# Kernel optimization log

Measured on AMD Instinct MI355X. Metric: run time of the kernel, lower is better.

Reference implementation:

```python
import jax, jax.numpy as jnp
import numpy as np

D_MODEL = 1024
N_HEADS = 16
D_FF = 4096
EPS = 1e-5


def setup_inputs() -> dict:
    key = jax.random.key(0)
    ks = jax.random.split(key, 10)
    sig_attn = (1.0 / D_MODEL) ** 0.5
    sig1 = (2.0 / (D_MODEL + D_FF)) ** 0.5
    sig2 = (2.0 / (D_FF + D_MODEL)) ** 0.5
    return {
        "x": jax.random.normal(ks[0], (4, 2048, D_MODEL), dtype=jnp.float32),
        "W_q": jax.random.normal(ks[1], (D_MODEL, D_MODEL), jnp.float32) * sig_attn,
        "W_k": jax.random.normal(ks[2], (D_MODEL, D_MODEL), jnp.float32) * sig_attn,
        "W_v": jax.random.normal(ks[3], (D_MODEL, D_MODEL), jnp.float32) * sig_attn,
        "W_o": jax.random.normal(ks[4], (D_MODEL, D_MODEL), jnp.float32) * sig_attn,
        "gamma1": jnp.ones((D_MODEL,), jnp.float32),
        "gamma2": jnp.ones((D_MODEL,), jnp.float32),
        "W1": jax.random.normal(ks[5], (D_FF, D_MODEL), jnp.float32) * sig1,  # gate proj
        "W2": jax.random.normal(ks[6], (D_MODEL, D_FF), jnp.float32) * sig2,  # down proj
        "W3": jax.random.normal(ks[7], (D_FF, D_MODEL), jnp.float32) * sig1,  # up proj
    }


def _rmsnorm(x, gamma, eps=EPS):
    # computed in fp32 as in the original, cast back to input dtype
    in_dtype = x.dtype
    xf = x.astype(jnp.float32)
    norm = jnp.sqrt(jnp.mean(xf * xf, axis=-1, keepdims=True) + eps)
    return ((xf / norm) * gamma).astype(in_dtype)


def _mha(x, W_q, W_k, W_v, W_o, n_heads=N_HEADS):
    B, S, D = x.shape
    d_h = D // n_heads
    # projections: weights stored as [d_out, d_in]
    q = jnp.einsum('bsd,ed->bse', x, W_q).reshape(B, S, n_heads, d_h).transpose(0, 2, 1, 3)
    k = jnp.einsum('bsd,ed->bse', x, W_k).reshape(B, S, n_heads, d_h).transpose(0, 2, 1, 3)
    v = jnp.einsum('bsd,ed->bse', x, W_v).reshape(B, S, n_heads, d_h).transpose(0, 2, 1, 3)
    scores = jnp.einsum('bhqd,bhkd->bhqk', q, k) / jnp.sqrt(jnp.asarray(d_h, x.dtype))
    causal = jnp.tril(jnp.ones((S, S), dtype=bool))  # True = keep
    scores = jnp.where(causal, scores, -jnp.inf)
    probs = jax.nn.softmax(scores, axis=-1)
    out = jnp.einsum('bhqk,bhkd->bhqd', probs, v)
    out = out.transpose(0, 2, 1, 3).reshape(B, S, D)
    return jnp.einsum('bse,de->bsd', out, W_o)


def _swiglu(x, W1, W2, W3):
    g = jnp.einsum('bsd,fd->bsf', x, W1)
    u = jnp.einsum('bsd,fd->bsf', x, W3)
    return jnp.einsum('bsf,df->bsd', jax.nn.silu(g) * u, W2)


def reference(x, W_q, W_k, W_v, W_o, gamma1, gamma2, W1, W2, W3):
    x = x + _mha(_rmsnorm(x, gamma1), W_q, W_k, W_v, W_o)
    x = x + _swiglu(_rmsnorm(x, gamma2), W1, W2, W3)
    return x
```

## Files before the change

kernel.cpp:

```cpp
#include <hip/hip_runtime.h>
#include <cstdint>
#include <cstddef>

typedef unsigned short u16;
typedef unsigned int u32;
typedef short bf16x8 __attribute__((ext_vector_type(8)));
typedef float f32x4 __attribute__((ext_vector_type(4)));
typedef float f32x16 __attribute__((ext_vector_type(16)));
typedef u16 u16x4 __attribute__((ext_vector_type(4)));

__device__ __forceinline__ u16 f2bf(float f) {
  u32 u = __float_as_uint(f);
  return (u16)((u + 0x7FFFu + ((u >> 16) & 1u)) >> 16);
}
__device__ __forceinline__ float bf2f(u16 h) {
  return __uint_as_float(((u32)h) << 16);
}
__device__ __forceinline__ u32 cvtpk(float lo, float hi) {
  u32 r;
  asm("v_cvt_pk_bf16_f32 %0, %1, %2" : "=v"(r) : "v"(lo), "v"(hi));
  return r;
}
__device__ __forceinline__ float exp2a(float x) {
  float r;
  asm("v_exp_f32 %0, %1" : "=v"(r) : "v"(x));
  return r;
}

__device__ __forceinline__ void gload_lds16(const void* g, void* l) {
  __builtin_amdgcn_global_load_lds((const __attribute__((address_space(1))) u32*)g,
                                   (__attribute__((address_space(3))) u32*)l, 16, 0, 0);
}

__global__ __launch_bounds__(256) void castw_multi(
    const float* __restrict__ Wq, const float* __restrict__ Wk,
    const float* __restrict__ Wv, const float* __restrict__ Wo,
    const float* __restrict__ W2, u16* __restrict__ qkvw,
    u16* __restrict__ Wo_b, u16* __restrict__ W2_b) {
  const int bid = blockIdx.x;
  const float* src;
  u16x4* dst;
  int i;
  if (bid < 3072) {
    src = (bid < 1024) ? Wq : (bid < 2048) ? Wk : Wv;
    dst = (u16x4*)qkvw + (bid >> 10) * 262144;
    i = (bid & 1023) * 256 + threadIdx.x;
  } else if (bid < 4096) {
    src = Wo;
    dst = (u16x4*)Wo_b;
    i = (bid - 3072) * 256 + threadIdx.x;
  } else {
    src = W2;
    dst = (u16x4*)W2_b;
    i = (bid - 4096) * 256 + threadIdx.x;
  }
  float4 v = ((const float4*)src)[i];
  u16x4 r;
  r.x = f2bf(v.x); r.y = f2bf(v.y); r.z = f2bf(v.z); r.w = f2bf(v.w);
  dst[i] = r;
}

__global__ __launch_bounds__(256) void castw_pack2(const float* __restrict__ W1,
                                                   const float* __restrict__ W3,
                                                   u16* __restrict__ dst) {
  const int half = blockIdx.y;
  const float* src = half ? W3 : W1;
  int i = blockIdx.x * 256 + threadIdx.x;
  float4 v = ((const float4*)src)[i];
  const int n = i >> 8;
  const int c4 = i & 255;
  const int orow = ((n >> 6) << 7) + (half << 6) + (n & 63);
  u16x4 r;
  r.x = f2bf(v.x); r.y = f2bf(v.y); r.z = f2bf(v.z); r.w = f2bf(v.w);
  ((u16x4*)dst)[orow * 256 + c4] = r;
}

__global__ __launch_bounds__(256) void rmsnorm_k(const float* __restrict__ x,
                                                 const float* __restrict__ gamma,
                                                 u16* __restrict__ o) {
  const int row = blockIdx.x;
  const int t = threadIdx.x;
  float4 v = ((const float4*)(x + (size_t)row * 1024))[t];
  float ss = v.x * v.x + v.y * v.y + v.z * v.z + v.w * v.w;
  #pragma unroll
  for (int m = 1; m < 64; m <<= 1) ss += __shfl_xor(ss, m);
  __shared__ float wsum[4];
  if ((t & 63) == 0) wsum[t >> 6] = ss;
  __syncthreads();
  float tot = wsum[0] + wsum[1] + wsum[2] + wsum[3];
  float inv = rsqrtf(tot * (1.0f / 1024.0f) + 1e-5f);
  float4 g = ((const float4*)gamma)[t];
  u16x4 r;
  r.x = f2bf(v.x * inv * g.x);
  r.y = f2bf(v.y * inv * g.y);
  r.z = f2bf(v.z * inv * g.z);
  r.w = f2bf(v.w * inv * g.w);
  ((u16x4*)(o + (size_t)row * 1024))[t] = r;
}

template <int EPI>
__global__ __launch_bounds__(256, 4)
void gemm128(const u16* __restrict__ A, const u16* __restrict__ B,
             void* out, const void* ep, int M, int N, int KLOOP, int KS,
             float scale, int ncut) {
  __shared__ u16 smem[2][8192];
  u16* const sA = smem[0];
  u16* const sB = smem[1];

  const int tid = threadIdx.x;
  const int lane = tid & 63;
  const int w = tid >> 6;
  const int wr = w >> 1, wc = w & 1;
  const int lr = lane & 15, lk = lane >> 4;

  A += (size_t)blockIdx.z * KLOOP;
  B += (size_t)blockIdx.z * KLOOP;

  const int nx = gridDim.x;
  const int nwg = nx * gridDim.y;
  const int flat = blockIdx.y * nx + blockIdx.x;
  const int qq = nwg >> 3, rr = nwg & 7;
  const int xcd = flat & 7, off = flat >> 3;
  const int swz = (xcd < rr ? xcd * (qq + 1) : rr * (qq + 1) + (xcd - rr) * qq) + off;
  const int sr = nx * 8;
  const int g8 = swz / sr, rem = swz % sr;
  const int grp = rem >> 6, r6 = rem & 63;
  const int m0 = (g8 * 8 + (r6 & 7)) * 128;
  const int n0 = (grp * 8 + (r6 >> 3)) * 128;

  f32x4 acc[4][4];
  #pragma unroll
  for (int i = 0; i < 4; i++)
    #pragma unroll
    for (int j = 0; j < 4; j++) acc[i][j] = (f32x4){0.f, 0.f, 0.f, 0.f};

  for (int kt = 0; kt < KLOOP; kt += 64) {
    __syncthreads();
    #pragma unroll
    for (int r = 0; r < 4; r++) {
      const int q = r * 256 + tid;
      const int row = q >> 3;
      const int cs = (q & 7) ^ (row & 7);
      gload_lds16(A + (size_t)(m0 + row) * KS + kt + cs * 8, (char*)sA + q * 16);
      gload_lds16(B + (size_t)(n0 + row) * KS + kt + cs * 8, (char*)sB + q * 16);
    }
    __syncthreads();
    #pragma unroll
    for (int kk = 0; kk < 2; kk++) {
      bf16x8 a_[4], b_[4];
      #pragma unroll
      for (int i = 0; i < 4; i++)
        a_[i] = *(const bf16x8*)&sA[(wr * 64 + i * 16 + lr) * 64 +
                                    (((kk * 4 + lk) ^ (lr & 7)) * 8)];
      #pragma unroll
      for (int j = 0; j < 4; j++)
        b_[j] = *(const bf16x8*)&sB[(wc * 64 + j * 16 + lr) * 64 +
                                    (((kk * 4 + lk) ^ (lr & 7)) * 8)];
      #pragma unroll
      for (int i = 0; i < 4; i++)
        #pragma unroll
        for (int j = 0; j < 4; j++)
          acc[i][j] = __builtin_amdgcn_mfma_f32_16x16x32_bf16(a_[i], b_[j], acc[i][j], 0, 0, 0);
    }
  }

  if constexpr (EPI == 1 || EPI == 3) {
    #pragma unroll
    for (int i = 0; i < 4; i++)
      #pragma unroll
      for (int j = 0; j < 4; j++)
        #pragma unroll
        for (int r = 0; r < 4; r++) {
          const int grow = m0 + wr * 64 + i * 16 + lk * 4 + r;
          const int gcol = n0 + wc * 64 + j * 16 + lr;
          const size_t idx = (size_t)grow * N + gcol;
          if (EPI == 1) ((float*)out)[idx] = ((const float*)ep)[idx] + acc[i][j][r];
          else          unsafeAtomicAdd((float*)out + idx, acc[i][j][r]);
        }
  } else {
    bool vpath = false;
    if constexpr (EPI == 5) vpath = (n0 >= 2048);
    if (vpath) {
      u16* const smT = smem[0];
      __syncthreads();
      #pragma unroll
      for (int i = 0; i < 4; i++)
        #pragma unroll
        for (int j = 0; j < 4; j++)
          #pragma unroll
          for (int r = 0; r < 4; r++) {
            const int row = wr * 64 + i * 16 + lk * 4 + r;
            const int col = wc * 64 + j * 16 + lr;
            smT[col * 128 + (row ^ ((col & 7) << 3))] = f2bf(acc[i][j][r]);
          }
      __syncthreads();
      u16* const vt = (u16*)const_cast<void*>(ep);
      const int b = m0 >> 11;
      const int sbase = m0 & 2047;
      #pragma unroll
      for (int it = 0; it < 8; it++) {
        const int fl = it * 256 + tid;
        const int trow = fl >> 4;
        const int tch = fl & 15;
        bf16x8 cv = *(const bf16x8*)&smT[trow * 128 + ((tch * 8) ^ ((trow & 7) << 3))];
        const int dg = n0 - 2048 + trow;
        const int h = dg >> 6, d = dg & 63;
        *(bf16x8*)(vt + (((size_t)(b * 16 + h) * 64 + d) * 2048 + sbase + tch * 8)) = cv;
      }
    } else {
      u16* const smC = smem[0];
      const float s = ((EPI == 0 || EPI == 5) && n0 < ncut) ? scale : 1.0f;
      __syncthreads();
      #pragma unroll
      for (int i = 0; i < 4; i++)
        #pragma unroll
        for (int j = 0; j < 4; j++)
          #pragma unroll
          for (int r = 0; r < 4; r++) {
            const int row = wr * 64 + i * 16 + lk * 4 + r;
            const int col = wc * 64 + j * 16 + lr;
            smC[row * 128 + (col ^ ((row & 7) << 3))] = f2bf(acc[i][j][r] * s);
          }
      __syncthreads();
      if constexpr (EPI == 4) {
        #pragma unroll
        for (int it = 0; it < 4; it++) {
          const int fl = it * 256 + tid;
          const int row = fl >> 3;
          const int ch = fl & 7;
          bf16x8 gvv = *(const bf16x8*)&smC[row * 128 + ((ch ^ (row & 7)) * 8)];
          bf16x8 uvv = *(const bf16x8*)&smC[row * 128 + (((ch + 8) ^ (row & 7)) * 8)];
          bf16x8 ov;
          #pragma unroll
          for (int k = 0; k < 8; k++) {
            float g = bf2f((u16)gvv[k]);
            float u = bf2f((u16)uvv[k]);
            float sg = g / (1.f + __expf(-g));
            ov[k] = (short)f2bf(sg * u);
          }
          *(bf16x8*)((u16*)out + (size_t)(m0 + row) * N + (n0 >> 1) + ch * 8) = ov;
        }
      } else {
        #pragma unroll
        for (int it = 0; it < 8; it++) {
          const int fl = it * 256 + tid;
          const int row = fl >> 4;
          const int ch = fl & 15;
          bf16x8 cv = *(const bf16x8*)&smC[row * 128 + ((ch ^ (row & 7)) * 8)];
          const size_t gidx = (size_t)(m0 + row) * N + n0 + ch * 8;
          *(bf16x8*)((u16*)out + gidx) = cv;
        }
      }
    }
  }
}

__global__ __launch_bounds__(256, 4)
void attn_fwd5(const u16* __restrict__ qkv, const u16* __restrict__ vt,
               u16* __restrict__ o) {
  __shared__ u16 sm[9216];
  u16* const smK = sm;
  u16* const smV = sm + 4096;

  const int tid = threadIdx.x;
  const int lane = tid & 63;
  const int w = tid >> 6;
  const int hi = lane >> 5;
  const int ln = lane & 31;

  const int flat = blockIdx.x;
  const int qt = 15 - (flat >> 6);
  const int bh = flat & 63;
  const int b = bh >> 4, h = bh & 15;

  const int qbase = qt * 128;
  const int qw0 = qbase + w * 32;
  const int qglob = qw0 + ln;
  const int nkb = qt * 2 + 2;

  bf16x8 qf[4];
  {
    const u16* qp = qkv + ((size_t)(b * 2048 + qw0 + ln)) * 3072 + h * 64 + hi * 8;
    #pragma unroll
    for (int c = 0; c < 4; c++) qf[c] = *(const bf16x8*)(qp + c * 16);
  }

  f32x16 accO[2];
  #pragma unroll
  for (int i = 0; i < 2; i++)
    #pragma unroll
    for (int r = 0; r < 16; r++) accO[i][r] = 0.f;
  float mrun = -1e30f, lsum = 0.f;

  for (int kb = 0; kb < nkb; kb++) {
    const int kbase = kb * 64;
    __syncthreads();
    #pragma unroll
    for (int r = 0; r < 2; r++) {
      const int cb = w * 128 + r * 64;
      const int ci = cb + lane;
      {
        const int key = ci >> 3, gch = (ci & 7) ^ (key & 7);
        const u16* src = qkv + ((size_t)(b * 2048 + kbase + key)) * 3072 + 1024 + h * 64 + gch * 8;
        gload_lds16(src, (char*)smK + cb * 16);
      }
      {
        const int d = ci >> 3, gch = (ci & 7) ^ (d & 7);
        const u16* src = vt + ((size_t)(bh * 64 + d)) * 2048 + kbase + gch * 8;
        gload_lds16(src, (char*)smV + cb * 16);
      }
    }
    __syncthreads();

    if (kbase <= qw0 + 31) {
      f32x16 st[2];
      #pragma unroll
      for (int kt = 0; kt < 2; kt++) {
        #pragma unroll
        for (int r = 0; r < 16; r++) st[kt][r] = 0.f;
      }
      __builtin_amdgcn_s_setprio(1);
      #pragma unroll
      for (int kt = 0; kt < 2; kt++)
        #pragma unroll
        for (int c = 0; c < 4; c++) {
          const int row = kt * 32 + ln;
          const int sch = (c * 2 + hi) ^ (ln & 7);
          bf16x8 kf = *(const bf16x8*)((const char*)smK + row * 128 + sch * 16);
          st[kt] = __builtin_amdgcn_mfma_f32_32x32x16_bf16(kf, qf[c], st[kt], 0, 0, 0);
        }
      __builtin_amdgcn_s_setprio(0);
      if (kbase + 63 > qw0) {
        #pragma unroll
        for (int kt = 0; kt < 2; kt++)
          #pragma unroll
          for (int r = 0; r < 16; r++) {
            const int kk = kbase + kt * 32 + (r & 3) + 8 * (r >> 2) + 4 * hi;
            if (kk > qglob) st[kt][r] = -1e30f;
          }
      }
      float t16[16];
      #pragma unroll
      for (int i = 0; i < 16; i++) t16[i] = fmaxf(st[0][i], st[1][i]);
      #pragma unroll
      for (int s = 8; s > 0; s >>= 1)
        #pragma unroll
        for (int i = 0; i < 8; i++)
          if (i < s) t16[i] = fmaxf(t16[i], t16[i + s]);
      float pm = t16[0];
      pm = fmaxf(pm, __shfl_xor(pm, 32));
      if (!__all(pm - mrun <= 8.f)) {
        const float mnew = fmaxf(mrun, pm);
        const float alpha = exp2a(mrun - mnew);
        lsum *= alpha;
        accO[0] *= alpha;
        accO[1] *= alpha;
        mrun = mnew;
      }
      #pragma unroll
      for (int kt = 0; kt < 2; kt++)
        #pragma unroll
        for (int r = 0; r < 16; r++) st[kt][r] = exp2a(st[kt][r] - mrun);
      float s16[16];
      #pragma unroll
      for (int i = 0; i < 16; i++) s16[i] = st[0][i] + st[1][i];
      #pragma unroll
      for (int s = 8; s > 0; s >>= 1)
        #pragma unroll
        for (int i = 0; i < 8; i++)
          if (i < s) s16[i] = s16[i] + s16[i + s];
      float ps = s16[0];
      ps += __shfl_xor(ps, 32);
      lsum += ps;

      #pragma unroll
      for (int kt = 0; kt < 2; kt++) {
        u32 pw[8], px[8];
        #pragma unroll
        for (int i = 0; i < 8; i++) pw[i] = cvtpk(st[kt][2 * i], st[kt][2 * i + 1]);
        #pragma unroll
        for (int i = 0; i < 8; i++) px[i] = (u32)__shfl_xor((int)pw[i], 32);
        union { u32 wd[4]; bf16x8 v; } f0, f1;
        f0.wd[0] = hi ? px[2] : pw[0];
        f0.wd[1] = hi ? px[3] : pw[1];
        f0.wd[2] = hi ? pw[2] : px[0];
        f0.wd[3] = hi ? pw[3] : px[1];
        f1.wd[0] = hi ? px[6] : pw[4];
        f1.wd[1] = hi ? px[7] : pw[5];
        f1.wd[2] = hi ? pw[6] : px[4];
        f1.wd[3] = hi ? pw[7] : px[5];
        __builtin_amdgcn_s_setprio(1);
        #pragma unroll
        for (int d0 = 0; d0 < 2; d0++) {
          #pragma unroll
          for (int kc = 0; kc < 2; kc++) {
            const int drow = d0 * 32 + ln;
            const int sch = (kt * 4 + kc * 2 + hi) ^ (ln & 7);
            bf16x8 vf = *(const bf16x8*)((const char*)smV + drow * 128 + sch * 16);
            accO[d0] = __builtin_amdgcn_mfma_f32_32x32x16_bf16(vf, kc ? f1.v : f0.v,
                                                               accO[d0], 0, 0, 0);
          }
        }
        __builtin_amdgcn_s_setprio(0);
      }
    }
  }

  __syncthreads();
  const float inv = 1.0f / lsum;
  #pragma unroll
  for (int d0 = 0; d0 < 2; d0++)
    #pragma unroll
    for (int r = 0; r < 16; r++) {
      const int d = d0 * 32 + (r & 3) + 8 * (r >> 2) + 4 * hi;
      sm[(w * 32 + ln) * 72 + d] = f2bf(accO[d0][r] * inv);
    }
  __syncthreads();
  const int ql = tid >> 1, dh = (tid & 1) * 32;
  const u16* srcp = &sm[ql * 72 + dh];
  u16* dst = o + ((size_t)(b * 2048 + qbase + ql)) * 1024 + h * 64 + dh;
  #pragma unroll
  for (int j = 0; j < 4; j++)
    *(bf16x8*)(dst + j * 8) = *(const bf16x8*)(srcp + j * 8);
}

extern "C" void kernel_launch(void* const* d_in, const int* in_sizes, int n_in,
                              void* d_out, int out_size, void* d_ws, size_t ws_size,
                              hipStream_t stream) {
  const float* x      = (const float*)d_in[0];
  const float* W_q    = (const float*)d_in[1];
  const float* W_k    = (const float*)d_in[2];
  const float* W_v    = (const float*)d_in[3];
  const float* W_o    = (const float*)d_in[4];
  const float* gamma1 = (const float*)d_in[5];
  const float* gamma2 = (const float*)d_in[6];
  const float* W1     = (const float*)d_in[7];
  const float* W2     = (const float*)d_in[8];
  const float* W3     = (const float*)d_in[9];

  char* ws = (char*)d_ws;
  const size_t MB = 1ull << 20;
  u16* qkvw  = (u16*)(ws + 0 * MB);
  u16* Wo_b  = (u16*)(ws + 6 * MB);
  u16* W13   = (u16*)(ws + 8 * MB);
  u16* W2_b  = (u16*)(ws + 24 * MB);
  u16* xn    = (u16*)(ws + 32 * MB);
  u16* qkvb  = (u16*)(ws + 48 * MB);
  u16* attnb = (u16*)(ws + 96 * MB);
  u16* vtb   = (u16*)(ws + 112 * MB);
  u16* hbuf  = (u16*)(ws + 128 * MB);
  float* x1  = (float*)d_out;

  castw_multi<<<8192, 256, 0, stream>>>(W_q, W_k, W_v, W_o, W2, qkvw, Wo_b, W2_b);
  castw_pack2<<<dim3(4096, 2), 256, 0, stream>>>(W1, W3, W13);

  rmsnorm_k<<<8192, 256, 0, stream>>>(x, gamma1, xn);
  gemm128<5><<<dim3(24, 64), 256, 0, stream>>>(xn, qkvw, qkvb, vtb,
                                               8192, 3072, 1024, 1024,
                                               0.125f * 1.44269504f, 1024);
  attn_fwd5<<<dim3(1024), 256, 0, stream>>>(qkvb, vtb, attnb);
  gemm128<1><<<dim3(8, 64), 256, 0, stream>>>(attnb, Wo_b, x1, x,
                                              8192, 1024, 1024, 1024, 1.0f, 0);

  rmsnorm_k<<<8192, 256, 0, stream>>>(x1, gamma2, xn);
  gemm128<4><<<dim3(64, 64), 256, 0, stream>>>(xn, W13, hbuf, nullptr,
                                               8192, 4096, 1024, 1024, 1.0f, 0);
  gemm128<3><<<dim3(8, 64, 2), 256, 0, stream>>>(hbuf, W2_b, (float*)d_out, nullptr,
                                                 8192, 1024, 2048, 4096, 1.0f, 0);
}
```

Baseline: 448.4 us.

## Fuse prep kernels, add double-buffered GEMM, drop split-K atomics for down-proj

Merges the weight casts, W1/W3 packing and the first RMSNorm into one launch to cut launch overhead. Adds a double-buffered LDS GEMM variant (two stages, occupancy hint of 2) for the two N=1024 output GEMMs. The down projection now runs the full K=4096 in one pass with a fused residual add instead of split-K atomic adds. This removes atomic traffic, but it halves the grid for that GEMM (512 blocks) and lowers occupancy.

```diff
diff --git a/kernel.cpp b/kernel.cpp
--- a/kernel.cpp
+++ b/kernel.cpp
@@ -32,47 +32,68 @@
                                    (__attribute__((address_space(3))) u32*)l, 16, 0, 0);
 }
 
-__global__ __launch_bounds__(256) void castw_multi(
+__global__ __launch_bounds__(256) void prep_all(
     const float* __restrict__ Wq, const float* __restrict__ Wk,
     const float* __restrict__ Wv, const float* __restrict__ Wo,
-    const float* __restrict__ W2, u16* __restrict__ qkvw,
-    u16* __restrict__ Wo_b, u16* __restrict__ W2_b) {
+    const float* __restrict__ W2, const float* __restrict__ W1,
+    const float* __restrict__ W3, const float* __restrict__ x,
+    const float* __restrict__ gamma1, u16* __restrict__ qkvw,
+    u16* __restrict__ Wo_b, u16* __restrict__ W2_b, u16* __restrict__ W13,
+    u16* __restrict__ xn) {
   const int bid = blockIdx.x;
-  const float* src;
-  u16x4* dst;
-  int i;
-  if (bid < 3072) {
-    src = (bid < 1024) ? Wq : (bid < 2048) ? Wk : Wv;
-    dst = (u16x4*)qkvw + (bid >> 10) * 262144;
-    i = (bid & 1023) * 256 + threadIdx.x;
-  } else if (bid < 4096) {
-    src = Wo;
-    dst = (u16x4*)Wo_b;
-    i = (bid - 3072) * 256 + threadIdx.x;
+  const int t = threadIdx.x;
+  if (bid < 8192) {
+    const float* src;
+    u16x4* dst;
+    int i;
+    if (bid < 3072) {
+      src = (bid < 1024) ? Wq : (bid < 2048) ? Wk : Wv;
+      dst = (u16x4*)qkvw + (bid >> 10) * 262144;
+      i = (bid & 1023) * 256 + t;
+    } else if (bid < 4096) {
+      src = Wo;
+      dst = (u16x4*)Wo_b;
+      i = (bid - 3072) * 256 + t;
+    } else {
+      src = W2;
+      dst = (u16x4*)W2_b;
+      i = (bid - 4096) * 256 + t;
+    }
+    float4 v = ((const float4*)src)[i];
+    u16x4 r;
+    r.x = f2bf(v.x); r.y = f2bf(v.y); r.z = f2bf(v.z); r.w = f2bf(v.w);
+    dst[i] = r;
+  } else if (bid < 16384) {
+    const int b2 = bid - 8192;
+    const int half = b2 >> 12;
+    const float* src = half ? W3 : W1;
+    int i = (b2 & 4095) * 256 + t;
+    float4 v = ((const float4*)src)[i];
+    const int n = i >> 8;
+    const int c4 = i & 255;
+    const int orow = ((n >> 6) << 7) + (half << 6) + (n & 63);
+    u16x4 r;
+    r.x = f2bf(v.x); r.y = f2bf(v.y); r.z = f2bf(v.z); r.w = f2bf(v.w);
+    ((u16x4*)W13)[orow * 256 + c4] = r;
   } else {
-    src = W2;
-    dst = (u16x4*)W2_b;
-    i = (bid - 4096) * 256 + threadIdx.x;
+    const int row = bid - 16384;
+    float4 v = ((const float4*)(x + (size_t)row * 1024))[t];
+    float ss = v.x * v.x + v.y * v.y + v.z * v.z + v.w * v.w;
+    #pragma unroll
+    for (int m = 1; m < 64; m <<= 1) ss += __shfl_xor(ss, m);
+    __shared__ float wsum[4];
+    if ((t & 63) == 0) wsum[t >> 6] = ss;
+    __syncthreads();
+    float tot = wsum[0] + wsum[1] + wsum[2] + wsum[3];
+    float inv = rsqrtf(tot * (1.0f / 1024.0f) + 1e-5f);
+    float4 g = ((const float4*)gamma1)[t];
+    u16x4 r;
+    r.x = f2bf(v.x * inv * g.x);
+    r.y = f2bf(v.y * inv * g.y);
+    r.z = f2bf(v.z * inv * g.z);
+    r.w = f2bf(v.w * inv * g.w);
+    ((u16x4*)(xn + (size_t)row * 1024))[t] = r;
   }
-  float4 v = ((const float4*)src)[i];
-  u16x4 r;
-  r.x = f2bf(v.x); r.y = f2bf(v.y); r.z = f2bf(v.z); r.w = f2bf(v.w);
-  dst[i] = r;
-}
-
-__global__ __launch_bounds__(256) void castw_pack2(const float* __restrict__ W1,
-                                                   const float* __restrict__ W3,
-                                                   u16* __restrict__ dst) {
-  const int half = blockIdx.y;
-  const float* src = half ? W3 : W1;
-  int i = blockIdx.x * 256 + threadIdx.x;
-  float4 v = ((const float4*)src)[i];
-  const int n = i >> 8;
-  const int c4 = i & 255;
-  const int orow = ((n >> 6) << 7) + (half << 6) + (n & 63);
-  u16x4 r;
-  r.x = f2bf(v.x); r.y = f2bf(v.y); r.z = f2bf(v.z); r.w = f2bf(v.w);
-  ((u16x4*)dst)[orow * 256 + c4] = r;
 }
 
 __global__ __launch_bounds__(256) void rmsnorm_k(const float* __restrict__ x,
@@ -113,9 +134,6 @@
   const int wr = w >> 1, wc = w & 1;
   const int lr = lane & 15, lk = lane >> 4;
 
-  A += (size_t)blockIdx.z * KLOOP;
-  B += (size_t)blockIdx.z * KLOOP;
-
   const int nx = gridDim.x;
   const int nwg = nx * gridDim.y;
   const int flat = blockIdx.y * nx + blockIdx.x;
@@ -164,95 +182,165 @@
     }
   }
 
-  if constexpr (EPI == 1 || EPI == 3) {
+  bool vpath = false;
+  if constexpr (EPI == 5) vpath = (n0 >= 2048);
+  if (vpath) {
+    u16* const smT = smem[0];
+    __syncthreads();
     #pragma unroll
     for (int i = 0; i < 4; i++)
       #pragma unroll
       for (int j = 0; j < 4; j++)
         #pragma unroll
         for (int r = 0; r < 4; r++) {
-          const int grow = m0 + wr * 64 + i * 16 + lk * 4 + r;
-          const int gcol = n0 + wc * 64 + j * 16 + lr;
-          const size_t idx = (size_t)grow * N + gcol;
-          if (EPI == 1) ((float*)out)[idx] = ((const float*)ep)[idx] + acc[i][j][r];
-          else          unsafeAtomicAdd((float*)out + idx, acc[i][j][r]);
+          const int row = wr * 64 + i * 16 + lk * 4 + r;
+          const int col = wc * 64 + j * 16 + lr;
+          smT[col * 128 + (row ^ ((col & 7) << 3))] = f2bf(acc[i][j][r]);
         }
+    __syncthreads();
+    u16* const vt = (u16*)const_cast<void*>(ep);
+    const int b = m0 >> 11;
+    const int sbase = m0 & 2047;
+    #pragma unroll
+    for (int it = 0; it < 8; it++) {
+      const int fl = it * 256 + tid;
+      const int trow = fl >> 4;
+      const int tch = fl & 15;
+      bf16x8 cv = *(const bf16x8*)&smT[trow * 128 + ((tch * 8) ^ ((trow & 7) << 3))];
+      const int dg = n0 - 2048 + trow;
+      const int h = dg >> 6, d = dg & 63;
+      *(bf16x8*)(vt + (((size_t)(b * 16 + h) * 64 + d) * 2048 + sbase + tch * 8)) = cv;
+    }
   } else {
-    bool vpath = false;
-    if constexpr (EPI == 5) vpath = (n0 >= 2048);
-    if (vpath) {
-      u16* const smT = smem[0];
-      __syncthreads();
-      #pragma unroll
-      for (int i = 0; i < 4; i++)
-        #pragma unroll
-        for (int j = 0; j < 4; j++)
-          #pragma unroll
-          for (int r = 0; r < 4; r++) {
-            const int row = wr * 64 + i * 16 + lk * 4 + r;
-            const int col = wc * 64 + j * 16 + lr;
-            smT[col * 128 + (row ^ ((col & 7) << 3))] = f2bf(acc[i][j][r]);
-          }
-      __syncthreads();
-      u16* const vt = (u16*)const_cast<void*>(ep);
-      const int b = m0 >> 11;
-      const int sbase = m0 & 2047;
+    u16* const smC = smem[0];
+    const float s = ((EPI == 0 || EPI == 5) && n0 < ncut) ? scale : 1.0f;
+    __syncthreads();
+    #pragma unroll
+    for (int i = 0; i < 4; i++)
+      #pragma unroll
+      for (int j = 0; j < 4; j++)
+        #pragma unroll
+        for (int r = 0; r < 4; r++) {
+          const int row = wr * 64 + i * 16 + lk * 4 + r;
+          const int col = wc * 64 + j * 16 + lr;
+          smC[row * 128 + (col ^ ((row & 7) << 3))] = f2bf(acc[i][j][r] * s);
+        }
+    __syncthreads();
+    if constexpr (EPI == 4) {
+      #pragma unroll
+      for (int it = 0; it < 4; it++) {
+        const int fl = it * 256 + tid;
+        const int row = fl >> 3;
+        const int ch = fl & 7;
+        bf16x8 gvv = *(const bf16x8*)&smC[row * 128 + ((ch ^ (row & 7)) * 8)];
+        bf16x8 uvv = *(const bf16x8*)&smC[row * 128 + (((ch + 8) ^ (row & 7)) * 8)];
+        bf16x8 ov;
+        #pragma unroll
+        for (int k = 0; k < 8; k++) {
+          float g = bf2f((u16)gvv[k]);
+          float u = bf2f((u16)uvv[k]);
+          float sg = g / (1.f + __expf(-g));
+          ov[k] = (short)f2bf(sg * u);
+        }
+        *(bf16x8*)((u16*)out + (size_t)(m0 + row) * N + (n0 >> 1) + ch * 8) = ov;
+      }
+    } else {
       #pragma unroll
       for (int it = 0; it < 8; it++) {
         const int fl = it * 256 + tid;
-        const int trow = fl >> 4;
-        const int tch = fl & 15;
-        bf16x8 cv = *(const bf16x8*)&smT[trow * 128 + ((tch * 8) ^ ((trow & 7) << 3))];
-        const int dg = n0 - 2048 + trow;
-        const int h = dg >> 6, d = dg & 63;
-        *(bf16x8*)(vt + (((size_t)(b * 16 + h) * 64 + d) * 2048 + sbase + tch * 8)) = cv;
-      }
-    } else {
-      u16* const smC = smem[0];
-      const float s = ((EPI == 0 || EPI == 5) && n0 < ncut) ? scale : 1.0f;
-      __syncthreads();
+        const int row = fl >> 4;
+        const int ch = fl & 15;
+        bf16x8 cv = *(const bf16x8*)&smC[row * 128 + ((ch ^ (row & 7)) * 8)];
+        const size_t gidx = (size_t)(m0 + row) * N + n0 + ch * 8;
+        *(bf16x8*)((u16*)out + gidx) = cv;
+      }
+    }
+  }
+}
+
+template <int EPI>
+__global__ __launch_bounds__(256, 2)
+void gemm128db(const u16* __restrict__ A, const u16* __restrict__ B,
+               void* out, const void* ep, int M, int N, int KLOOP, int KS,
+               float scale, int ncut) {
+  __shared__ u16 sA[2][8192];
+  __shared__ u16 sB[2][8192];
+
+  const int tid = threadIdx.x;
+  const int lane = tid & 63;
+  const int w = tid >> 6;
+  const int wr = w >> 1, wc = w & 1;
+  const int lr = lane & 15, lk = lane >> 4;
+
+  const int nx = gridDim.x;
+  const int nwg = nx * gridDim.y;
+  const int flat = blockIdx.y * nx + blockIdx.x;
+  const int qq = nwg >> 3, rr = nwg & 7;
+  const int xcd = flat & 7, off = flat >> 3;
+  const int swz = (xcd < rr ? xcd * (qq + 1) : rr * (qq + 1) + (xcd - rr) * qq) + off;
+  const int sr = nx * 8;
+  const int g8 = swz / sr, rem = swz % sr;
+  const int grp = rem >> 6, r6 = rem & 63;
+  const int m0 = (g8 * 8 + (r6 & 7)) * 128;
+  const int n0 = (grp * 8 + (r6 >> 3)) * 128;
+
+  f32x4 acc[4][4];
+  #pragma unroll
+  for (int i = 0; i < 4; i++)
+    #pragma unroll
+    for (int j = 0; j < 4; j++) acc[i][j] = (f32x4){0.f, 0.f, 0.f, 0.f};
+
+  #define STAGE128(BUF, KT)                                                       \
+    _Pragma("unroll")                                                             \
+    for (int r = 0; r < 4; r++) {                                                 \
+      const int q = r * 256 + tid;                                                \
+      const int row = q >> 3;                                                     \
+      const int cs = (q & 7) ^ (row & 7);                                         \
+      gload_lds16(A + (size_t)(m0 + row) * KS + (KT) + cs * 8,                    \
+                  (char*)sA[BUF] + q * 16);                                       \
+      gload_lds16(B + (size_t)(n0 + row) * KS + (KT) + cs * 8,                    \
+                  (char*)sB[BUF] + q * 16);                                       \
+    }
+
+  const int NT = KLOOP >> 6;
+  STAGE128(0, 0)
+  __syncthreads();
+
+  for (int W = 0; W < NT; ++W) {
+    const int buf = W & 1;
+    if (W + 1 < NT) { STAGE128(buf ^ 1, (W + 1) << 6) }
+    #pragma unroll
+    for (int kk = 0; kk < 2; kk++) {
+      bf16x8 a_[4], b_[4];
       #pragma unroll
       for (int i = 0; i < 4; i++)
+        a_[i] = *(const bf16x8*)&sA[buf][(wr * 64 + i * 16 + lr) * 64 +
+                                        (((kk * 4 + lk) ^ (lr & 7)) * 8)];
+      #pragma unroll
+      for (int j = 0; j < 4; j++)
+        b_[j] = *(const bf16x8*)&sB[buf][(wc * 64 + j * 16 + lr) * 64 +
+                                         (((kk * 4 + lk) ^ (lr & 7)) * 8)];
+      #pragma unroll
+      for (int i = 0; i < 4; i++)
         #pragma unroll
         for (int j = 0; j < 4; j++)
-          #pragma unroll
-          for (int r = 0; r < 4; r++) {
-            const int row = wr * 64 + i * 16 + lk * 4 + r;
-            const int col = wc * 64 + j * 16 + lr;
-            smC[row * 128 + (col ^ ((row & 7) << 3))] = f2bf(acc[i][j][r] * s);
-          }
-      __syncthreads();
-      if constexpr (EPI == 4) {
-        #pragma unroll
-        for (int it = 0; it < 4; it++) {
-          const int fl = it * 256 + tid;
-          const int row = fl >> 3;
-          const int ch = fl & 7;
-          bf16x8 gvv = *(const bf16x8*)&smC[row * 128 + ((ch ^ (row & 7)) * 8)];
-          bf16x8 uvv = *(const bf16x8*)&smC[row * 128 + (((ch + 8) ^ (row & 7)) * 8)];
-          bf16x8 ov;
-          #pragma unroll
-          for (int k = 0; k < 8; k++) {
-            float g = bf2f((u16)gvv[k]);
-            float u = bf2f((u16)uvv[k]);
-            float sg = g / (1.f + __expf(-g));
-            ov[k] = (short)f2bf(sg * u);
-          }
-          *(bf16x8*)((u16*)out + (size_t)(m0 + row) * N + (n0 >> 1) + ch * 8) = ov;
-        }
-      } else {
-        #pragma unroll
-        for (int it = 0; it < 8; it++) {
-          const int fl = it * 256 + tid;
-          const int row = fl >> 4;
-          const int ch = fl & 15;
-          bf16x8 cv = *(const bf16x8*)&smC[row * 128 + ((ch ^ (row & 7)) * 8)];
-          const size_t gidx = (size_t)(m0 + row) * N + n0 + ch * 8;
-          *(bf16x8*)((u16*)out + gidx) = cv;
-        }
-      }
-    }
+          acc[i][j] = __builtin_amdgcn_mfma_f32_16x16x32_bf16(a_[i], b_[j], acc[i][j], 0, 0, 0);
+    }
+    __syncthreads();
   }
+  #undef STAGE128
+
+  #pragma unroll
+  for (int i = 0; i < 4; i++)
+    #pragma unroll
+    for (int j = 0; j < 4; j++)
+      #pragma unroll
+      for (int r = 0; r < 4; r++) {
+        const int grow = m0 + wr * 64 + i * 16 + lk * 4 + r;
+        const int gcol = n0 + wc * 64 + j * 16 + lr;
+        const size_t idx = (size_t)grow * N + gcol;
+        ((float*)out)[idx] = ((const float*)ep)[idx] + acc[i][j][r];
+      }
 }
 
 __global__ __launch_bounds__(256, 4)
@@ -451,20 +539,20 @@
   u16* hbuf  = (u16*)(ws + 128 * MB);
   float* x1  = (float*)d_out;
 
-  castw_multi<<<8192, 256, 0, stream>>>(W_q, W_k, W_v, W_o, W2, qkvw, Wo_b, W2_b);
-  castw_pack2<<<dim3(4096, 2), 256, 0, stream>>>(W1, W3, W13);
-
-  rmsnorm_k<<<8192, 256, 0, stream>>>(x, gamma1, xn);
+  prep_all<<<24576, 256, 0, stream>>>(W_q, W_k, W_v, W_o, W2, W1, W3, x, gamma1,
+                                      qkvw, Wo_b, W2_b, W13, xn);
+
   gemm128<5><<<dim3(24, 64), 256, 0, stream>>>(xn, qkvw, qkvb, vtb,
                                                8192, 3072, 1024, 1024,
                                                0.125f * 1.44269504f, 1024);
   attn_fwd5<<<dim3(1024), 256, 0, stream>>>(qkvb, vtb, attnb);
-  gemm128<1><<<dim3(8, 64), 256, 0, stream>>>(attnb, Wo_b, x1, x,
-                                              8192, 1024, 1024, 1024, 1.0f, 0);
+  gemm128db<1><<<dim3(8, 64), 256, 0, stream>>>(attnb, Wo_b, x1, x,
+                                                8192, 1024, 1024, 1024, 1.0f, 0);
 
   rmsnorm_k<<<8192, 256, 0, stream>>>(x1, gamma2, xn);
   gemm128<4><<<dim3(64, 64), 256, 0, stream>>>(xn, W13, hbuf, nullptr,
                                                8192, 4096, 1024, 1024, 1.0f, 0);
-  gemm128<3><<<dim3(8, 64, 2), 256, 0, stream>>>(hbuf, W2_b, (float*)d_out, nullptr,
-                                                 8192, 1024, 2048, 4096, 1.0f, 0);
-}
+  gemm128db<1><<<dim3(8, 64), 256, 0, stream>>>(hbuf, W2_b, (float*)d_out,
+                                                (const float*)d_out,
+                                                8192, 1024, 4096, 4096, 1.0f, 0);
+}
```

After: 442.1 us, median of 2. Within noise of the previous version (-1.4%).
